# Kernel optimization log

Measured on AMD Instinct MI355X. Metric: run time of the kernel, lower is better.

The kernel has to match this reference:

```python
import jax, jax.numpy as jnp
import numpy as np

SIGMA = 1e-4   # SoftRas coverage sharpness
GAMMA = 0.1    # depth-softmax temperature
IMAGE_SIZE = 128


def _normalize(v):
    return v / (jnp.linalg.norm(v, axis=-1, keepdims=True) + 1e-8)


def _look_at(eye, center, up):
    z = _normalize(eye - center)
    x = _normalize(jnp.cross(up, z))
    y = jnp.cross(z, x)
    R = jnp.stack([x, y, z], axis=-2)                       # (B,3,3)
    t = -jnp.einsum('bij,bj->bi', R, eye)
    B = eye.shape[0]
    M = jnp.tile(jnp.eye(4, dtype=eye.dtype), (B, 1, 1))
    M = M.at[:, :3, :3].set(R).at[:, :3, 3].set(t)
    return M


def _perspective(fov_y, aspect, near, far):
    f = 1.0 / np.tan(fov_y / 2.0)
    M = np.zeros((4, 4), np.float32)
    M[0, 0] = f / aspect
    M[1, 1] = f
    M[2, 2] = (far + near) / (near - far)
    M[2, 3] = 2.0 * far * near / (near - far)
    M[3, 2] = -1.0
    return jnp.asarray(M)


def _project(verts_world, eye, center, up):
    B, V, _ = verts_world.shape
    view = _look_at(eye, center, up)
    proj = _perspective(np.deg2rad(60.0), 1.0, 0.1, 10.0)
    M = jnp.einsum('ij,bjk->bik', proj, view)
    vh = jnp.concatenate([verts_world, jnp.ones((B, V, 1), verts_world.dtype)], -1)
    clip = jnp.einsum('bij,bvj->bvi', M, vh)
    return clip[..., :3] / (clip[..., 3:4] + 1e-8)            # (B,V,3) NDC


def _edge_dist(p, a, b):
    # p: (H,W,2); a,b: (B,F,2) -> unsigned point-to-segment distance (B,F,H,W)
    pa = p[None, None] - a[:, :, None, None]                  # (B,F,H,W,2)
    ba = (b - a)[:, :, None, None]                            # (B,F,1,1,2)
    t = jnp.clip(jnp.sum(pa * ba, -1) / (jnp.sum(ba * ba, -1) + 1e-12), 0.0, 1.0)
    d = pa - t[..., None] * ba
    return jnp.sqrt(jnp.sum(d * d, -1) + 1e-12)


def _cross2(u, v):
    return u[..., 0] * v[..., 1] - u[..., 1] * v[..., 0]


def _rasterize(verts_ndc, faces, colors, image_size):
    tri = verts_ndc[:, faces]                                 # (B,F,3,3)
    v2, vz = tri[..., :2], tri[..., 2]                        # (B,F,3,2), (B,F,3)
    xs = (jnp.arange(image_size) + 0.5) / image_size * 2.0 - 1.0
    ys = 1.0 - (jnp.arange(image_size) + 0.5) / image_size * 2.0
    X, Y = jnp.meshgrid(xs, ys, indexing='xy')
    p = jnp.stack([X, Y], -1)                                 # (H,W,2)

    a0, a1, a2 = v2[:, :, 0], v2[:, :, 1], v2[:, :, 2]        # (B,F,2)
    area = _cross2(a1 - a0, a2 - a0)[:, :, None, None]        # (B,F,1,1)
    denom = area + jnp.where(area >= 0, 1e-12, -1e-12)
    w0 = _cross2((a2 - a1)[:, :, None, None], p[None, None] - a1[:, :, None, None])
    w1 = _cross2((a0 - a2)[:, :, None, None], p[None, None] - a2[:, :, None, None])
    w2 = _cross2((a1 - a0)[:, :, None, None], p[None, None] - a0[:, :, None, None])
    b0, b1, b2 = w0 / denom, w1 / denom, w2 / denom           # barycentrics (B,F,H,W)
    inside = (b0 >= 0) & (b1 >= 0) & (b2 >= 0)

    d = jnp.minimum(jnp.minimum(_edge_dist(p, a0, a1), _edge_dist(p, a1, a2)),
                    _edge_dist(p, a2, a0))
    sgn = jnp.where(inside, 1.0, -1.0)
    prob = jax.nn.sigmoid(sgn * d * d / SIGMA)                # soft coverage (B,F,H,W)
    sil = 1.0 - jnp.prod(1.0 - prob, axis=1, keepdims=True)   # (B,1,H,W)

    bc0, bc1, bc2 = (jnp.clip(b0, 0., 1.), jnp.clip(b1, 0., 1.), jnp.clip(b2, 0., 1.))
    s = bc0 + bc1 + bc2 + 1e-8
    zpix = (bc0 * vz[:, :, 0, None, None] + bc1 * vz[:, :, 1, None, None]
            + bc2 * vz[:, :, 2, None, None]) / s
    zn = jnp.clip((1.0 - zpix) * 0.5, 0.0, 1.0)               # 1 = near
    m = jnp.max(zn, axis=1, keepdims=True)
    Dw = prob * jnp.exp((zn - m) / GAMMA)
    w_bg = jnp.exp((0.0 - m) / GAMMA)                         # background (far, black)
    Wn = Dw / (jnp.sum(Dw, axis=1, keepdims=True) + w_bg)     # (B,F,H,W)
    face_col = jnp.mean(colors[:, faces], axis=2)             # (B,F,3)
    rgb = jnp.einsum('bfhw,bfc->bchw', Wn, face_col)          # (B,3,H,W)
    return sil, rgb


def setup_inputs() -> dict:
    key = jax.random.key(0)
    k1, k2, k3, k4 = jax.random.split(key, 4)
    B, V, F = 4, 256, 256
    verts_world = jax.random.normal(k1, (B, V, 3), jnp.float32) * 0.5
    faces = jax.random.randint(k2, (F, 3), 0, V)
    colors = jax.random.uniform(k3, (B, V, 3), jnp.float32)
    eye = jnp.tile(jnp.array([0.0, 0.0, 2.5], jnp.float32), (B, 1)) \
          + jax.random.normal(k4, (B, 3), jnp.float32) * 0.05
    return {"verts_world": verts_world, "faces": faces, "colors": colors, "eye": eye}


def reference(verts_world, faces, colors, eye):
    B = verts_world.shape[0]
    center = jnp.zeros((B, 3), verts_world.dtype)
    up = jnp.tile(jnp.array([0.0, 1.0, 0.0], verts_world.dtype), (B, 1))
    verts_ndc = _project(verts_world, eye, center, up)
    return _rasterize(verts_ndc, faces, colors, IMAGE_SIZE)
```

## Files before the change

kernel.cpp:

```cpp
#include <hip/hip_runtime.h>

#define NB 4
#define NV 256
#define NF 256
#define IMG 128
#define STR 32

typedef float v2f __attribute__((ext_vector_type(2)));
typedef float v4f __attribute__((ext_vector_type(4)));

__device__ __forceinline__ float rcpf(float x) { return __builtin_amdgcn_rcpf(x); }
__device__ __forceinline__ float ex2(float x)  { return __builtin_amdgcn_exp2f(x); }
__device__ __forceinline__ float med01(float x) { return __builtin_amdgcn_fmed3f(x, 0.0f, 1.0f); }
__device__ __forceinline__ v2f med01_2(v2f v) { return (v2f){ med01(v.x), med01(v.y) }; }
__device__ __forceinline__ v2f fma2(v2f a, v2f b, v2f c) { return __builtin_elementwise_fma(a, b, c); }
__device__ __forceinline__ v2f lo2(v4f q) { return __builtin_shufflevector(q, q, 0, 1); }
__device__ __forceinline__ v2f hi2(v4f q) { return __builtin_shufflevector(q, q, 2, 3); }

#define SCV   120.11224139682566f
#define ISC2  6.931471805599453e-05f
#define KGAMV 14.426950408889634f


__global__ void prep_faces(const float* __restrict__ verts,
                           const int* __restrict__ faces,
                           const float* __restrict__ colors,
                           const float* __restrict__ eye,
                           float* __restrict__ ws)
{
    const int b = blockIdx.x;
    const int f = threadIdx.x;

    const float fpj = 1.7320508075688772f;
    const float p22 = -1.0202020202020203f;
    const float p23 = -0.20202020202020202f;

    float ex = eye[b*3+0], ey = eye[b*3+1], ez = eye[b*3+2];
    float en  = sqrtf(ex*ex + ey*ey + ez*ez);
    float izn = 1.0f / (en + 1e-8f);
    float zx = ex*izn, zy = ey*izn, zz = ez*izn;
    float cn  = sqrtf(zz*zz + zx*zx);
    float ixn = 1.0f / (cn + 1e-8f);
    float xx = zz*ixn, xy = 0.0f, xz = -zx*ixn;
    float yx = zy*xz - zz*xy;
    float yy = zz*xx - zx*xz;
    float yz = zx*xy - zy*xx;
    float tx = -(xx*ex + xy*ey + xz*ez);
    float ty = -(yx*ex + yy*ey + yz*ez);
    float tz = -(zx*ex + zy*ey + zz*ez);

    int i0 = faces[f*3+0], i1 = faces[f*3+1], i2 = faces[f*3+2];
    int idx[3] = { i0, i1, i2 };

    float ax[3], ay[3], az[3];
#pragma unroll
    for (int k = 0; k < 3; ++k) {
        const float* v = verts + (b*NV + idx[k])*3;
        float vx = v[0], vy = v[1], vz = v[2];
        float cx  = fpj*(xx*vx + xy*vy + xz*vz + tx);
        float cyv = fpj*(yx*vx + yy*vy + yz*vz + ty);
        float zv  = zx*vx + zy*vy + zz*vz + tz;
        float cz  = p22*zv + p23;
        float cw  = -zv;
        float iw  = 1.0f / (cw + 1e-8f);
        ax[k] = cx*iw; ay[k] = cyv*iw; az[k] = cz*iw;
    }

    float a0x = ax[0], a0y = ay[0];
    float a1x = ax[1], a1y = ay[1];
    float a2x = ax[2], a2y = ay[2];

    float e01x = a1x - a0x, e01y = a1y - a0y;
    float e12x = a2x - a1x, e12y = a2y - a1y;
    float e20x = a0x - a2x, e20y = a0y - a2y;

    float area  = e01x*(a2y - a0y) - e01y*(a2x - a0x);
    float denom = area + (area >= 0.0f ? 1e-12f : -1e-12f);
    float idn   = 1.0f / denom;

    float ib01 = 1.0f / (e01x*e01x + e01y*e01y + 1e-12f);
    float ib12 = 1.0f / (e12x*e12x + e12y*e12y + 1e-12f);
    float ib20 = 1.0f / (e20x*e20x + e20y*e20y + 1e-12f);

    const float third = (1.0f/3.0f);
    float cr = (colors[(b*NV+i0)*3+0] + colors[(b*NV+i1)*3+0] + colors[(b*NV+i2)*3+0]) * third;
    float cg = (colors[(b*NV+i0)*3+1] + colors[(b*NV+i1)*3+1] + colors[(b*NV+i2)*3+1]) * third;
    float cb = (colors[(b*NV+i0)*3+2] + colors[(b*NV+i1)*3+2] + colors[(b*NV+i2)*3+2]) * third;

    float* o = ws + (b*128 + (f >> 1))*STR + (f & 1);
    o[ 0]=a0x*SCV;   o[ 2]=a0y*SCV;
    o[ 4]=e01x*SCV;  o[ 6]=e01y*SCV;
    o[ 8]=e12x*SCV;  o[10]=e12y*SCV;
    o[12]=ib01*ISC2; o[14]=ib12*ISC2; o[16]=ib20*ISC2;
    o[18]=idn*ISC2;
    o[20]=az[0]; o[22]=az[1]; o[24]=az[2];
    o[26]=cr;   o[28]=cg;   o[30]=cb;
}

__launch_bounds__(512, 4)
__global__ void raster(const float* __restrict__ ws, float* __restrict__ out)
{
    __shared__ float sFD[4096];

    const int t   = threadIdx.x;
    const int cy  = threadIdx.y;
    const int bid = blockIdx.x;
    const int b    = bid >> 8;
    const int tile = bid & 255;
    const int tx0 = (tile & 15) << 3;
    const int ty0 = (tile >> 4) << 3;

    {
        const float4* src = (const float4*)(ws + (b << 12));
        float4* dst = (float4*)sFD;
        int tid = (cy << 6) + t;
        dst[tid]       = src[tid];
        dst[tid + 512] = src[tid + 512];
    }
    __syncthreads();

    const int w = tx0 + (t & 7);
    const int h = ty0 + (t >> 3);
    const float xs = ((w + 0.5f) * (1.0f/64.0f) - 1.0f) * SCV;
    const float ys = (1.0f - (h + 0.5f) * (1.0f/64.0f)) * SCV;
    const v2f PX = { xs, xs }, PY = { ys, ys };

    const v2f KGH_NEG = { -0.5f*KGAMV, -0.5f*KGAMV };
    const v2f KGH_POS = {  0.5f*KGAMV,  0.5f*KGAMV };
    const v2f ONE2 = { 1.0f, 1.0f };
    const v2f EPS2 = { 1e-8f, 1e-8f };

    const float* fc = sFD + (cy << 4)*STR;

    v2f aP = ONE2, aS = {0,0}, aR0 = {0,0}, aR1 = {0,0}, aR2 = {0,0};

#pragma unroll
    for (int i = 0; i < 16; ++i) {
        const float* c = fc + i*STR;
        v4f q0 = *(const v4f*)(c +  0);
        v4f q1 = *(const v4f*)(c +  4);
        v4f q2 = *(const v4f*)(c +  8);
        v4f q3 = *(const v4f*)(c + 12);
        v4f q4 = *(const v4f*)(c + 16);
        v4f q5 = *(const v4f*)(c + 20);
        v4f q6 = *(const v4f*)(c + 24);
        v4f q7 = *(const v4f*)(c + 28);
        v2f a0x = lo2(q0), a0y = hi2(q0);
        v2f e01x = lo2(q1), e01y = hi2(q1);
        v2f e12x = lo2(q2), e12y = hi2(q2);
        v2f ib01 = lo2(q3), ib12 = hi2(q3);
        v2f ib20 = lo2(q4), idn  = hi2(q4);
        v2f z0 = lo2(q5), z1 = hi2(q5);
        v2f z2 = lo2(q6), cr = hi2(q6);
        v2f cg = lo2(q7), cb = hi2(q7);

        v2f e20x = -(e01x + e12x), e20y = -(e01y + e12y);
        v2f g01x = e01x*ib01, g01y = e01y*ib01;
        v2f g12x = e12x*ib12, g12y = e12y*ib12;
        v2f g20x = e20x*ib20, g20y = e20y*ib20;

        v2f pa0x = PX - a0x, pa0y = PY - a0y;
        v2f pa1x = pa0x - e01x, pa1y = pa0y - e01y;
        v2f pa2x = pa0x + e20x, pa2y = pa0y + e20y;
        v2f b0 = fma2(-e12y, pa1x, e12x*pa1y) * idn;
        v2f b1 = fma2(-e20y, pa2x, e20x*pa2y) * idn;
        v2f b2 = (ONE2 - b0) - b1;

        v2f tt = med01_2(fma2(pa0x, g01x, pa0y*g01y));
        v2f dx = fma2(-tt, e01x, pa0x);
        v2f dy = fma2(-tt, e01y, pa0y);
        v2f ddA = fma2(dx, dx, dy*dy);
        tt = med01_2(fma2(pa1x, g12x, pa1y*g12y));
        dx = fma2(-tt, e12x, pa1x);
        dy = fma2(-tt, e12y, pa1y);
        v2f ddB = fma2(dx, dx, dy*dy);
        tt = med01_2(fma2(pa2x, g20x, pa2y*g20y));
        dx = fma2(-tt, e20x, pa2x);
        dy = fma2(-tt, e20y, pa2y);
        v2f ddC = fma2(dx, dx, dy*dy);

        v2f dd = __builtin_elementwise_min(__builtin_elementwise_min(ddA, ddB), ddC);
        v2f mx = __builtin_elementwise_max(__builtin_elementwise_max(-b0, -b1), -b2);
        v2f q  = { copysignf(dd.x, mx.x), copysignf(dd.y, mx.y) };

        v2f e2 = { ex2(q.x), ex2(q.y) };
        v2f den = e2 + ONE2;
        v2f prob = { rcpf(den.x), rcpf(den.y) };
        aP = fma2(-prob, aP, aP);

        v2f bc0 = med01_2(b0), bc1 = med01_2(b1), bc2 = med01_2(b2);
        v2f s = (bc0 + bc1) + (bc2 + EPS2);
        v2f zs = fma2(bc0, z0, fma2(bc1, z1, bc2*z2));
        v2f irs = { rcpf(s.x), rcpf(s.y) };
        v2f zq = fma2(zs*irs, KGH_NEG, KGH_POS);
        v2f ez = { ex2(__builtin_amdgcn_fmed3f(zq.x, 0.0f, KGAMV)),
                   ex2(__builtin_amdgcn_fmed3f(zq.y, 0.0f, KGAMV)) };
        v2f wgt = prob * ez;
        aS  = aS + wgt;
        aR0 = fma2(wgt, cr, aR0);
        aR1 = fma2(wgt, cg, aR1);
        aR2 = fma2(wgt, cb, aR2);
    }

    __syncthreads();
    float* red = sFD;
    red[(0*8 + cy)*64 + t] = aP.x * aP.y;
    red[(1*8 + cy)*64 + t] = aS.x + aS.y;
    red[(2*8 + cy)*64 + t] = aR0.x + aR0.y;
    red[(3*8 + cy)*64 + t] = aR1.x + aR1.y;
    red[(4*8 + cy)*64 + t] = aR2.x + aR2.y;
    __syncthreads();

    if (cy == 0) {
        float P = 1.0f, St = 0.0f, r0 = 0.0f, r1 = 0.0f, r2 = 0.0f;
#pragma unroll
        for (int c2 = 0; c2 < 8; ++c2) {
            P  *= red[(0*8 + c2)*64 + t];
            St += red[(1*8 + c2)*64 + t];
            r0 += red[(2*8 + c2)*64 + t];
            r1 += red[(3*8 + c2)*64 + t];
            r2 += red[(4*8 + c2)*64 + t];
        }
        float iden = rcpf(St + 1.0f);

        const int pix = h*IMG + w;
        out[b*16384 + pix] = 1.0f - P;
        float* rgb = out + 65536;
        rgb[(b*3 + 0)*16384 + pix] = r0 * iden;
        rgb[(b*3 + 1)*16384 + pix] = r1 * iden;
        rgb[(b*3 + 2)*16384 + pix] = r2 * iden;
    }
}

extern "C" void kernel_launch(void* const* d_in, const int* in_sizes, int n_in,
                              void* d_out, int out_size, void* d_ws, size_t ws_size,
                              hipStream_t stream)
{
    const float* verts  = (const float*)d_in[0];
    const int*   faces  = (const int*)d_in[1];
    const float* colors = (const float*)d_in[2];
    const float* eye    = (const float*)d_in[3];
    float* out = (float*)d_out;
    float* ws  = (float*)d_ws;

    hipLaunchKernelGGL(prep_faces, dim3(4),    dim3(256),   0, stream,
                       verts, faces, colors, eye, ws);
    hipLaunchKernelGGL(raster,     dim3(1024), dim3(64, 8), 0, stream, ws, out);
}
```

Before: 33.35 us.

## Read per-face data via scalar constant loads instead of LDS staging

The raster kernel no longer stages face data into shared memory. Each wave instead reads its 32 faces through a constant-address-space pointer, so the loads become wave-uniform scalar loads. The face record is repacked one face per 32-float record, with more values precomputed in prep (a1, a2, e20, edge gradients, idn-scaled edges), which removes per-pixel work from the inner loop. The packed-pair v2f math is dropped for scalar code, and the pixel mapping changes from 8x8 tiles to rows. The trade-offs are the loss of packed FMA throughput and a reliance on the scalar cache.

```diff
diff --git a/kernel.cpp b/kernel.cpp
--- a/kernel.cpp
+++ b/kernel.cpp
@@ -4,21 +4,15 @@
 #define NV 256
 #define NF 256
 #define IMG 128
-#define STR 32
-
-typedef float v2f __attribute__((ext_vector_type(2)));
-typedef float v4f __attribute__((ext_vector_type(4)));
+#define FSTR 32
+
+#define CONST_AS __attribute__((address_space(4)))
 
 __device__ __forceinline__ float rcpf(float x) { return __builtin_amdgcn_rcpf(x); }
 __device__ __forceinline__ float ex2(float x)  { return __builtin_amdgcn_exp2f(x); }
 __device__ __forceinline__ float med01(float x) { return __builtin_amdgcn_fmed3f(x, 0.0f, 1.0f); }
-__device__ __forceinline__ v2f med01_2(v2f v) { return (v2f){ med01(v.x), med01(v.y) }; }
-__device__ __forceinline__ v2f fma2(v2f a, v2f b, v2f c) { return __builtin_elementwise_fma(a, b, c); }
-__device__ __forceinline__ v2f lo2(v4f q) { return __builtin_shufflevector(q, q, 0, 1); }
-__device__ __forceinline__ v2f hi2(v4f q) { return __builtin_shufflevector(q, q, 2, 3); }
 
 #define SCV   120.11224139682566f
-#define ISC2  6.931471805599453e-05f
 #define KGAMV 14.426950408889634f
 
 
@@ -87,135 +81,106 @@
     float cg = (colors[(b*NV+i0)*3+1] + colors[(b*NV+i1)*3+1] + colors[(b*NV+i2)*3+1]) * third;
     float cb = (colors[(b*NV+i0)*3+2] + colors[(b*NV+i1)*3+2] + colors[(b*NV+i2)*3+2]) * third;
 
-    float* o = ws + (b*128 + (f >> 1))*STR + (f & 1);
-    o[ 0]=a0x*SCV;   o[ 2]=a0y*SCV;
-    o[ 4]=e01x*SCV;  o[ 6]=e01y*SCV;
-    o[ 8]=e12x*SCV;  o[10]=e12y*SCV;
-    o[12]=ib01*ISC2; o[14]=ib12*ISC2; o[16]=ib20*ISC2;
-    o[18]=idn*ISC2;
-    o[20]=az[0]; o[22]=az[1]; o[24]=az[2];
-    o[26]=cr;   o[28]=cg;   o[30]=cb;
+    const float ISC = 1.0f / SCV;
+
+    float* o = ws + ((b << 8) + f)*FSTR;
+    o[ 0]=a0x*SCV;  o[ 1]=a0y*SCV;
+    o[ 2]=a1x*SCV;  o[ 3]=a1y*SCV;
+    o[ 4]=a2x*SCV;  o[ 5]=a2y*SCV;
+    o[ 6]=e01x*SCV; o[ 7]=e01y*SCV;
+    o[ 8]=e12x*SCV; o[ 9]=e12y*SCV;
+    o[10]=e20x*SCV; o[11]=e20y*SCV;
+    o[12]=e01x*ib01*ISC; o[13]=e01y*ib01*ISC;
+    o[14]=e12x*ib12*ISC; o[15]=e12y*ib12*ISC;
+    o[16]=e20x*ib20*ISC; o[17]=e20y*ib20*ISC;
+    o[18]=e12x*idn*ISC;  o[19]=e12y*idn*ISC;
+    o[20]=e20x*idn*ISC;  o[21]=e20y*idn*ISC;
+    o[22]=az[0]; o[23]=az[1]; o[24]=az[2];
+    o[25]=cr;    o[26]=cg;    o[27]=cb;
+    o[28]=0.0f;  o[29]=0.0f;  o[30]=0.0f;  o[31]=0.0f;
 }
 
 __launch_bounds__(512, 4)
 __global__ void raster(const float* __restrict__ ws, float* __restrict__ out)
 {
-    __shared__ float sFD[4096];
+    __shared__ float red[5*8*64];
 
     const int t   = threadIdx.x;
     const int cy  = threadIdx.y;
     const int bid = blockIdx.x;
-    const int b    = bid >> 8;
-    const int tile = bid & 255;
-    const int tx0 = (tile & 15) << 3;
-    const int ty0 = (tile >> 4) << 3;
-
-    {
-        const float4* src = (const float4*)(ws + (b << 12));
-        float4* dst = (float4*)sFD;
-        int tid = (cy << 6) + t;
-        dst[tid]       = src[tid];
-        dst[tid + 512] = src[tid + 512];
+    const int b   = bid >> 8;
+    const int grp = bid & 255;
+    const int pix = grp*64 + t;
+    const int h = pix >> 7;
+    const int w = pix & 127;
+
+    const float pxs = ((w + 0.5f) * (1.0f/64.0f) - 1.0f) * SCV;
+    const float pys = (1.0f - (h + 0.5f) * (1.0f/64.0f)) * SCV;
+
+    const CONST_AS float* fc =
+        (const CONST_AS float*)(unsigned long long)(ws + (((b << 8) + (cy << 5)) << 5));
+
+    float P = 1.0f, S = 0.0f, R0 = 0.0f, R1 = 0.0f, R2 = 0.0f;
+
+#pragma unroll 4
+    for (int i = 0; i < 32; ++i) {
+        const CONST_AS float* c = fc + (i << 5);
+
+        float pa0x = pxs - c[0], pa0y = pys - c[1];
+        float pa1x = pxs - c[2], pa1y = pys - c[3];
+        float pa2x = pxs - c[4], pa2y = pys - c[5];
+
+        float b0 = fmaf(c[18], pa1y, -(c[19]*pa1x));
+        float b1 = fmaf(c[20], pa2y, -(c[21]*pa2x));
+        float b2 = (1.0f - b0) - b1;
+
+        float tt = med01(fmaf(c[12], pa0x, c[13]*pa0y));
+        float dx = fmaf(-tt, c[6], pa0x);
+        float dy = fmaf(-tt, c[7], pa0y);
+        float dd0 = fmaf(dx, dx, dy*dy);
+
+        tt = med01(fmaf(c[14], pa1x, c[15]*pa1y));
+        dx = fmaf(-tt, c[8], pa1x);
+        dy = fmaf(-tt, c[9], pa1y);
+        float dd1 = fmaf(dx, dx, dy*dy);
+
+        tt = med01(fmaf(c[16], pa2x, c[17]*pa2y));
+        dx = fmaf(-tt, c[10], pa2x);
+        dy = fmaf(-tt, c[11], pa2y);
+        float dd2 = fmaf(dx, dx, dy*dy);
+
+        float dd = fminf(fminf(dd0, dd1), dd2);
+        float mx = fmaxf(fmaxf(-b0, -b1), -b2);
+        float q  = copysignf(dd, mx);
+
+        float prob = rcpf(1.0f + ex2(q));
+        P = fmaf(-prob, P, P);
+
+        float bc0 = med01(b0), bc1 = med01(b1), bc2 = med01(b2);
+        float s  = (bc0 + bc1) + bc2;
+        float zs = fmaf(c[24], bc2, fmaf(c[23], bc1, bc0*c[22]));
+        float zq = fmaf(zs * rcpf(s), -0.5f*KGAMV, 0.5f*KGAMV);
+        float ez = ex2(__builtin_amdgcn_fmed3f(zq, 0.0f, KGAMV));
+        float wgt = prob * ez;
+
+        S += wgt;
+        R0 = fmaf(wgt, c[25], R0);
+        R1 = fmaf(wgt, c[26], R1);
+        R2 = fmaf(wgt, c[27], R2);
     }
+
+    red[(0*8 + cy)*64 + t] = P;
+    red[(1*8 + cy)*64 + t] = S;
+    red[(2*8 + cy)*64 + t] = R0;
+    red[(3*8 + cy)*64 + t] = R1;
+    red[(4*8 + cy)*64 + t] = R2;
     __syncthreads();
 
-    const int w = tx0 + (t & 7);
-    const int h = ty0 + (t >> 3);
-    const float xs = ((w + 0.5f) * (1.0f/64.0f) - 1.0f) * SCV;
-    const float ys = (1.0f - (h + 0.5f) * (1.0f/64.0f)) * SCV;
-    const v2f PX = { xs, xs }, PY = { ys, ys };
-
-    const v2f KGH_NEG = { -0.5f*KGAMV, -0.5f*KGAMV };
-    const v2f KGH_POS = {  0.5f*KGAMV,  0.5f*KGAMV };
-    const v2f ONE2 = { 1.0f, 1.0f };
-    const v2f EPS2 = { 1e-8f, 1e-8f };
-
-    const float* fc = sFD + (cy << 4)*STR;
-
-    v2f aP = ONE2, aS = {0,0}, aR0 = {0,0}, aR1 = {0,0}, aR2 = {0,0};
-
-#pragma unroll
-    for (int i = 0; i < 16; ++i) {
-        const float* c = fc + i*STR;
-        v4f q0 = *(const v4f*)(c +  0);
-        v4f q1 = *(const v4f*)(c +  4);
-        v4f q2 = *(const v4f*)(c +  8);
-        v4f q3 = *(const v4f*)(c + 12);
-        v4f q4 = *(const v4f*)(c + 16);
-        v4f q5 = *(const v4f*)(c + 20);
-        v4f q6 = *(const v4f*)(c + 24);
-        v4f q7 = *(const v4f*)(c + 28);
-        v2f a0x = lo2(q0), a0y = hi2(q0);
-        v2f e01x = lo2(q1), e01y = hi2(q1);
-        v2f e12x = lo2(q2), e12y = hi2(q2);
-        v2f ib01 = lo2(q3), ib12 = hi2(q3);
-        v2f ib20 = lo2(q4), idn  = hi2(q4);
-        v2f z0 = lo2(q5), z1 = hi2(q5);
-        v2f z2 = lo2(q6), cr = hi2(q6);
-        v2f cg = lo2(q7), cb = hi2(q7);
-
-        v2f e20x = -(e01x + e12x), e20y = -(e01y + e12y);
-        v2f g01x = e01x*ib01, g01y = e01y*ib01;
-        v2f g12x = e12x*ib12, g12y = e12y*ib12;
-        v2f g20x = e20x*ib20, g20y = e20y*ib20;
-
-        v2f pa0x = PX - a0x, pa0y = PY - a0y;
-        v2f pa1x = pa0x - e01x, pa1y = pa0y - e01y;
-        v2f pa2x = pa0x + e20x, pa2y = pa0y + e20y;
-        v2f b0 = fma2(-e12y, pa1x, e12x*pa1y) * idn;
-        v2f b1 = fma2(-e20y, pa2x, e20x*pa2y) * idn;
-        v2f b2 = (ONE2 - b0) - b1;
-
-        v2f tt = med01_2(fma2(pa0x, g01x, pa0y*g01y));
-        v2f dx = fma2(-tt, e01x, pa0x);
-        v2f dy = fma2(-tt, e01y, pa0y);
-        v2f ddA = fma2(dx, dx, dy*dy);
-        tt = med01_2(fma2(pa1x, g12x, pa1y*g12y));
-        dx = fma2(-tt, e12x, pa1x);
-        dy = fma2(-tt, e12y, pa1y);
-        v2f ddB = fma2(dx, dx, dy*dy);
-        tt = med01_2(fma2(pa2x, g20x, pa2y*g20y));
-        dx = fma2(-tt, e20x, pa2x);
-        dy = fma2(-tt, e20y, pa2y);
-        v2f ddC = fma2(dx, dx, dy*dy);
-
-        v2f dd = __builtin_elementwise_min(__builtin_elementwise_min(ddA, ddB), ddC);
-        v2f mx = __builtin_elementwise_max(__builtin_elementwise_max(-b0, -b1), -b2);
-        v2f q  = { copysignf(dd.x, mx.x), copysignf(dd.y, mx.y) };
-
-        v2f e2 = { ex2(q.x), ex2(q.y) };
-        v2f den = e2 + ONE2;
-        v2f prob = { rcpf(den.x), rcpf(den.y) };
-        aP = fma2(-prob, aP, aP);
-
-        v2f bc0 = med01_2(b0), bc1 = med01_2(b1), bc2 = med01_2(b2);
-        v2f s = (bc0 + bc1) + (bc2 + EPS2);
-        v2f zs = fma2(bc0, z0, fma2(bc1, z1, bc2*z2));
-        v2f irs = { rcpf(s.x), rcpf(s.y) };
-        v2f zq = fma2(zs*irs, KGH_NEG, KGH_POS);
-        v2f ez = { ex2(__builtin_amdgcn_fmed3f(zq.x, 0.0f, KGAMV)),
-                   ex2(__builtin_amdgcn_fmed3f(zq.y, 0.0f, KGAMV)) };
-        v2f wgt = prob * ez;
-        aS  = aS + wgt;
-        aR0 = fma2(wgt, cr, aR0);
-        aR1 = fma2(wgt, cg, aR1);
-        aR2 = fma2(wgt, cb, aR2);
-    }
-
-    __syncthreads();
-    float* red = sFD;
-    red[(0*8 + cy)*64 + t] = aP.x * aP.y;
-    red[(1*8 + cy)*64 + t] = aS.x + aS.y;
-    red[(2*8 + cy)*64 + t] = aR0.x + aR0.y;
-    red[(3*8 + cy)*64 + t] = aR1.x + aR1.y;
-    red[(4*8 + cy)*64 + t] = aR2.x + aR2.y;
-    __syncthreads();
-
     if (cy == 0) {
-        float P = 1.0f, St = 0.0f, r0 = 0.0f, r1 = 0.0f, r2 = 0.0f;
+        float Pt = 1.0f, St = 0.0f, r0 = 0.0f, r1 = 0.0f, r2 = 0.0f;
 #pragma unroll
         for (int c2 = 0; c2 < 8; ++c2) {
-            P  *= red[(0*8 + c2)*64 + t];
+            Pt *= red[(0*8 + c2)*64 + t];
             St += red[(1*8 + c2)*64 + t];
             r0 += red[(2*8 + c2)*64 + t];
             r1 += red[(3*8 + c2)*64 + t];
@@ -223,8 +188,7 @@
         }
         float iden = rcpf(St + 1.0f);
 
-        const int pix = h*IMG + w;
-        out[b*16384 + pix] = 1.0f - P;
+        out[b*16384 + pix] = 1.0f - Pt;
         float* rgb = out + 65536;
         rgb[(b*3 + 0)*16384 + pix] = r0 * iden;
         rgb[(b*3 + 1)*16384 + pix] = r1 * iden;
```

Measured after the change: 63.39 us. 90.1% more time.
